# Optimization experiments

Hardware: AMD Instinct MI355X
Metric: run time of the kernel (lower is better)

## Reference

```python
import jax, jax.numpy as jnp
import numpy as np

N = 100000        # nodes
E = 1600000       # edges (N * avg_degree 16)
D_IN = 128
D_OUT = 32
OBS_T = 60        # observation_time -> decay table size 60*OBS_T = 3600
T_MAX = 60 * OBS_T


def setup_inputs() -> dict:
    key = jax.random.key(0)
    ks = jax.random.split(key, 8)
    inp = {
        "input": jax.random.normal(ks[0], (N, D_IN), dtype=jnp.float32),
        "W": jax.random.normal(ks[1], (D_IN, D_OUT), dtype=jnp.float32) * (np.sqrt(2.0) / np.sqrt(D_IN)),
        # decay weights are abs(normal(0, 0.02)) in the original; rand*0.04 is same scale
        "decay_weight1": jnp.abs(jax.random.normal(ks[2], (T_MAX, 1), dtype=jnp.float32) * 0.02),
        "decay_weight2": jnp.abs(jax.random.normal(ks[3], (T_MAX, 1), dtype=jnp.float32) * 0.02),
        "edge_row": jax.random.randint(ks[4], (E,), 0, N, dtype=jnp.int32),
        "edge_col": jax.random.randint(ks[5], (E,), 0, N, dtype=jnp.int32),
        # zero-based interval index; equals (adj_value - 1) of the original code
        "edge_time": jax.random.randint(ks[6], (E,), 0, T_MAX, dtype=jnp.int32),
        "arrive_time": jax.random.randint(ks[7], (N,), 0, T_MAX, dtype=jnp.int32),
        "observation_time": OBS_T,
    }
    return inp


def reference(input, W, decay_weight1, decay_weight2,
              edge_row, edge_col, edge_time, arrive_time, observation_time):
    n_nodes = input.shape[0]
    # h = relu(input @ W)  [N, D_OUT]
    h = jax.nn.relu(jnp.matmul(input, W))
    # one-hot(interval) @ decay_weight1 == embedding lookup  -> per-edge decay scalar
    decay = decay_weight1[edge_time, 0]                        # [E]
    # SpecialSpmm: out[i] = sum_{edges (i,j)} decay_e * h[j]  (gather-scale-scatter)
    msgs = decay[:, None] * h[edge_col]                        # [E, D_OUT]
    h_prime = jax.ops.segment_sum(msgs, edge_row, num_segments=n_nodes)
    # outlayer window decay: one-hot(60*T - arrive - 1) @ decay_weight2 == lookup
    win_idx = 60 * observation_time - arrive_time - 1          # [N] in [0, 60*T)
    h_prime = decay_weight2[win_idx, 0][:, None] * h_prime
    return h_prime
```

## Files before the change

### kernel.cpp

```cpp
#include <hip/hip_runtime.h>

#define N_NODES 100000
#define N_EDGES 1600000
#define D_IN    128
#define D_OUT   32
#define RPB     8
#define NB      (N_NODES / RPB)
#define CROWS   2048
#define NCB     49
#define FPC     (CROWS / RPB)
#define NSH     8
#define CAP_A   4500
#define DEPTH   48
#define CAPF    200
#define GEMM_BLKS ((N_NODES + 63) / 64)
#define GRID_A  2048
#define EPB_A   ((N_EDGES + GRID_A - 1) / GRID_A)

typedef __attribute__((ext_vector_type(8))) short bf16x8;
typedef __attribute__((ext_vector_type(4))) float f32x4;

__device__ inline short f2bf(float f) {
    union { float f; unsigned u; } v; v.f = f;
    unsigned r = (v.u + 0x7FFFu + ((v.u >> 16) & 1u)) >> 16;
    return (short)r;
}
__device__ inline float bf2f(unsigned short b) {
    return __uint_as_float((unsigned)b << 16);
}

union SMemGA {
    struct { short wbt[D_IN * D_OUT]; } g;
    struct { uint2 lbin[NCB][DEPTH]; int lcnt[NCB]; int gbase[NCB]; } a;
};

__global__ __launch_bounds__(256) void gemm_phaseA_kernel(
    const float* __restrict__ input, const float* __restrict__ W,
    const int* __restrict__ erow,    const int* __restrict__ ecol,
    const int* __restrict__ etime,
    unsigned short* __restrict__ h16,
    int* __restrict__ gcur,
    uint2* __restrict__ segA)
{
    __shared__ SMemGA sm;
    const int tid = threadIdx.x;

    if (blockIdx.x < GEMM_BLKS) {
        for (int i = tid; i < D_IN * D_OUT; i += 256) {
            const int k = i >> 5, c = i & 31;
            sm.g.wbt[c * D_IN + k] = f2bf(W[i]);
        }
        __syncthreads();

        const int wave = tid >> 6;
        const int lane = tid & 63;
        const int r0   = blockIdx.x * 64 + wave * 16;
        const int c16  = lane & 15;
        const int quad = lane >> 4;

        int ra = r0 + c16;
        if (ra >= N_NODES) ra = N_NODES - 1;
        const float* arow = input + (size_t)ra * D_IN;

        f32x4 acc0 = {0.f, 0.f, 0.f, 0.f};
        f32x4 acc1 = {0.f, 0.f, 0.f, 0.f};
#pragma unroll
        for (int q = 0; q < 4; ++q) {
            const float* ap = arow + q * 32 + quad * 8;
            f32x4 a0 = *(const f32x4*)(ap);
            f32x4 a1 = *(const f32x4*)(ap + 4);
            bf16x8 af;
            af[0] = f2bf(a0.x); af[1] = f2bf(a0.y); af[2] = f2bf(a0.z); af[3] = f2bf(a0.w);
            af[4] = f2bf(a1.x); af[5] = f2bf(a1.y); af[6] = f2bf(a1.z); af[7] = f2bf(a1.w);
            bf16x8 b0 = *(const bf16x8*)(sm.g.wbt + (c16)      * D_IN + q * 32 + quad * 8);
            bf16x8 b1 = *(const bf16x8*)(sm.g.wbt + (c16 + 16) * D_IN + q * 32 + quad * 8);
            acc0 = __builtin_amdgcn_mfma_f32_16x16x32_bf16(af, b0, acc0, 0, 0, 0);
            acc1 = __builtin_amdgcn_mfma_f32_16x16x32_bf16(af, b1, acc1, 0, 0, 0);
        }
#pragma unroll
        for (int i = 0; i < 4; ++i) {
            const int rr = r0 + quad * 4 + i;
            if (rr < N_NODES) {
                h16[(size_t)rr * D_OUT + c16]      = (unsigned short)f2bf(fmaxf(acc0[i], 0.f));
                h16[(size_t)rr * D_OUT + c16 + 16] = (unsigned short)f2bf(fmaxf(acc1[i], 0.f));
            }
        }
    } else {
        const int blk   = blockIdx.x - GEMM_BLKS;
        const int shard = blk & (NSH - 1);
        const int wv    = tid >> 6;
        const int ln    = tid & 63;

        if (tid < NCB) sm.a.lcnt[tid] = 0;
        __syncthreads();

        const int e_beg = blk * EPB_A;
        const int e_end = min(e_beg + EPB_A, N_EDGES);

        for (int e = e_beg + tid; e < e_end; e += 256) {
            const int row = erow[e];
            const int cb  = row >> 11;
            uint2 p;
            p.x = (unsigned)ecol[e] | ((unsigned)(row & (CROWS - 1)) << 17);
            p.y = (unsigned)etime[e];
            const int pos = atomicAdd(&sm.a.lcnt[cb], 1);
            if (pos < DEPTH) sm.a.lbin[cb][pos] = p;
            else {
                const int gp = atomicAdd(&gcur[(cb * NSH + shard) * 16], 1);
                if (gp < CAP_A) segA[(size_t)(cb * NSH + shard) * CAP_A + gp] = p;
            }
        }
        __syncthreads();

        if (tid < NCB) {
            const int c = min(sm.a.lcnt[tid], DEPTH);
            sm.a.gbase[tid] = atomicAdd(&gcur[(tid * NSH + shard) * 16], c);
        }
        __syncthreads();

        for (int bin = wv; bin < NCB; bin += 4) {
            const int c  = min(sm.a.lcnt[bin], DEPTH);
            const int gb = sm.a.gbase[bin];
            uint2* seg = segA + (size_t)(bin * NSH + shard) * CAP_A;
            for (int k = ln; k < c; k += 64)
                if (gb + k < CAP_A) seg[gb + k] = sm.a.lbin[bin][k];
        }
    }
}

__global__ __launch_bounds__(256) void phaseB_kernel(
    const int* __restrict__ gcur, const uint2* __restrict__ segA,
    int* __restrict__ fcur,
    unsigned* __restrict__ spk2)
{
    __shared__ int hist[FPC];
    __shared__ int curs[FPC];

    const int tid    = threadIdx.x;
    const int seg_id = blockIdx.x >> 1;
    const int half   = blockIdx.x & 1;
    const int cb     = seg_id >> 3;
    const int shard  = seg_id & 7;
    const int ntot   = min(gcur[(cb * NSH + shard) * 16], CAP_A);
    const int nh     = (ntot + 1) >> 1;
    const int beg    = half * nh;
    const int end    = min(ntot, beg + nh);
    const uint2* seg = segA + (size_t)(cb * NSH + shard) * CAP_A;

    hist[tid] = 0;
    __syncthreads();

    for (int i = beg + tid; i < end; i += 256)
        atomicAdd(&hist[(seg[i].x >> 20) & 255], 1);
    __syncthreads();

    {
        const int h  = hist[tid];
        const int fb = cb * FPC + tid;
        curs[tid] = (h && fb < NB) ? atomicAdd(&fcur[fb], h) : 0;
    }
    __syncthreads();

    for (int i = beg + tid; i < end; i += 256) {
        const uint2 p   = seg[i];
        const unsigned crl = (p.x >> 17) & 2047u;
        const int      fl  = crl >> 3;
        const unsigned rec = (p.x & 0x1FFFFu) | ((crl & 7u) << 17) | (p.y << 20);
        const int pos = atomicAdd(&curs[fl], 1);
        if (pos < CAPF)
            spk2[(size_t)(cb * FPC + fl) * CAPF + pos] = rec;
    }
}

__global__ __launch_bounds__(256) void bucket_reduce_kernel(
    const unsigned short* __restrict__ h16, const int* __restrict__ fcur,
    const unsigned* __restrict__ spk2, const float* __restrict__ dw1,
    const float* __restrict__ dw2, const int* __restrict__ arrive,
    const int* __restrict__ obs, float* __restrict__ out)
{
    __shared__ unsigned pk[CAPF];
    __shared__ unsigned pks[CAPF];
    __shared__ int bin[RPB];
    __shared__ int start[RPB + 1];
    __shared__ int cur[RPB];

    const int tid = threadIdx.x;
    const int b   = blockIdx.x;
    const int n   = min(fcur[b], CAPF);
    const unsigned* seg = spk2 + (size_t)b * CAPF;

    if (tid < RPB) bin[tid] = 0;
    __syncthreads();

    for (int i = tid; i < n; i += 256) {
        const unsigned p = seg[i];
        pk[i] = p;
        atomicAdd(&bin[(p >> 17) & 7], 1);
    }
    __syncthreads();

    if (tid == 0) {
        int a = 0;
#pragma unroll
        for (int r = 0; r < RPB; ++r) { start[r] = a; cur[r] = a; a += bin[r]; }
        start[RPB] = a;
    }
    __syncthreads();

    for (int i = tid; i < n; i += 256) {
        const unsigned p = pk[i];
        pks[atomicAdd(&cur[(p >> 17) & 7], 1)] = p;
    }
    __syncthreads();

    const int c = tid & 31;
    const int g = tid >> 5;
    const int T = 60 * obs[0];

    const int beg = start[g];
    const int end = start[g + 1];

    float acc = 0.f;
    int j = beg;
    for (; j + 8 <= end; j += 8) {
        float a0 = 0.f, a1 = 0.f;
#pragma unroll
        for (int u = 0; u < 8; u += 2) {
            const unsigned pa = pks[j + u];
            const unsigned pb = pks[j + u + 1];
            const float va = bf2f(h16[(size_t)(pa & 0x1FFFF) * D_OUT + c]);
            const float vb = bf2f(h16[(size_t)(pb & 0x1FFFF) * D_OUT + c]);
            a0 = fmaf(dw1[pa >> 20], va, a0);
            a1 = fmaf(dw1[pb >> 20], vb, a1);
        }
        acc += a0 + a1;
    }
    for (; j < end; ++j) {
        const unsigned p = pks[j];
        acc = fmaf(dw1[p >> 20],
                   bf2f(h16[(size_t)(p & 0x1FFFF) * D_OUT + c]), acc);
    }

    const int r = b * RPB + g;
    const float sdw = dw2[T - arrive[r] - 1];
    out[(size_t)r * D_OUT + c] = acc * sdw;
}

extern "C" void kernel_launch(void* const* d_in, const int* in_sizes, int n_in,
                              void* d_out, int out_size, void* d_ws, size_t ws_size,
                              hipStream_t stream)
{
    const float* input  = (const float*)d_in[0];
    const float* W      = (const float*)d_in[1];
    const float* dw1    = (const float*)d_in[2];
    const float* dw2    = (const float*)d_in[3];
    const int*   erow   = (const int*)d_in[4];
    const int*   ecol   = (const int*)d_in[5];
    const int*   etime  = (const int*)d_in[6];
    const int*   arrive = (const int*)d_in[7];
    const int*   obs    = (const int*)d_in[8];

    float* out = (float*)d_out;

    char* p = (char*)d_ws;
    unsigned short* h16 = (unsigned short*)p;
    p += (size_t)N_NODES * D_OUT * 2;
    p = (char*)(((size_t)p + 255) & ~(size_t)255);
    int* gcur = (int*)p;
    p += (size_t)NCB * NSH * 16 * 4;
    int* fcur = (int*)p;
    p += (size_t)NB * 4;
    p = (char*)(((size_t)p + 255) & ~(size_t)255);
    uint2* segA = (uint2*)p;
    p += (size_t)NCB * NSH * CAP_A * 8;
    p = (char*)(((size_t)p + 255) & ~(size_t)255);
    unsigned* spk2 = (unsigned*)p;

    hipMemsetAsync(gcur, 0, (size_t)(NCB * NSH * 16 + NB) * 4, stream);

    gemm_phaseA_kernel<<<GEMM_BLKS + GRID_A, 256, 0, stream>>>(
        input, W, erow, ecol, etime, h16, gcur, segA);
    phaseB_kernel<<<NCB * NSH * 2, 256, 0, stream>>>(gcur, segA, fcur, spk2);
    bucket_reduce_kernel<<<NB, 256, 0, stream>>>(
        h16, fcur, spk2, dw1, dw2, arrive, obs, out);
}
```

Before: 185.9 us.

## Replace two-phase edge binning with direct global-atomic scatter into row buckets

Removes the shared-memory coarse binning pass and the separate phaseB kernel, and instead scatters each edge straight into its 8-row bucket using one global atomicAdd per edge. GEMM and scatter blocks are now interleaved (even and odd block indices) in one launch, which drops a kernel launch and the intermediate segA buffer round trip. The cost is 1.6M global atomics spread over 12.5K counters, which may contend or serialize more than the hierarchical scheme did. GEMM_BLKS equals SCAT_BLKS (1563), so the even/odd split covers both parts exactly.

```diff
diff --git a/kernel.cpp b/kernel.cpp
--- a/kernel.cpp
+++ b/kernel.cpp
@@ -6,16 +6,10 @@
 #define D_OUT   32
 #define RPB     8
 #define NB      (N_NODES / RPB)
-#define CROWS   2048
-#define NCB     49
-#define FPC     (CROWS / RPB)
-#define NSH     8
-#define CAP_A   4500
-#define DEPTH   48
 #define CAPF    200
 #define GEMM_BLKS ((N_NODES + 63) / 64)
-#define GRID_A  2048
-#define EPB_A   ((N_EDGES + GRID_A - 1) / GRID_A)
+#define EPB_S   1024
+#define SCAT_BLKS ((N_EDGES + EPB_S - 1) / EPB_S)
 
 typedef __attribute__((ext_vector_type(8))) short bf16x8;
 typedef __attribute__((ext_vector_type(4))) float f32x4;
@@ -29,32 +23,28 @@
     return __uint_as_float((unsigned)b << 16);
 }
 
-union SMemGA {
-    struct { short wbt[D_IN * D_OUT]; } g;
-    struct { uint2 lbin[NCB][DEPTH]; int lcnt[NCB]; int gbase[NCB]; } a;
-};
-
-__global__ __launch_bounds__(256) void gemm_phaseA_kernel(
+__global__ __launch_bounds__(256) void gemm_scatter_kernel(
     const float* __restrict__ input, const float* __restrict__ W,
     const int* __restrict__ erow,    const int* __restrict__ ecol,
     const int* __restrict__ etime,
     unsigned short* __restrict__ h16,
-    int* __restrict__ gcur,
-    uint2* __restrict__ segA)
+    int* __restrict__ fcur,
+    unsigned* __restrict__ spk2)
 {
-    __shared__ SMemGA sm;
+    __shared__ short wbt[D_IN * D_OUT];
     const int tid = threadIdx.x;
 
-    if (blockIdx.x < GEMM_BLKS) {
+    if ((blockIdx.x & 1) == 0) {
+        const int gblk = blockIdx.x >> 1;
         for (int i = tid; i < D_IN * D_OUT; i += 256) {
             const int k = i >> 5, c = i & 31;
-            sm.g.wbt[c * D_IN + k] = f2bf(W[i]);
+            wbt[c * D_IN + k] = f2bf(W[i]);
         }
         __syncthreads();
 
         const int wave = tid >> 6;
         const int lane = tid & 63;
-        const int r0   = blockIdx.x * 64 + wave * 16;
+        const int r0   = gblk * 64 + wave * 16;
         const int c16  = lane & 15;
         const int quad = lane >> 4;
 
@@ -72,8 +62,8 @@
             bf16x8 af;
             af[0] = f2bf(a0.x); af[1] = f2bf(a0.y); af[2] = f2bf(a0.z); af[3] = f2bf(a0.w);
             af[4] = f2bf(a1.x); af[5] = f2bf(a1.y); af[6] = f2bf(a1.z); af[7] = f2bf(a1.w);
-            bf16x8 b0 = *(const bf16x8*)(sm.g.wbt + (c16)      * D_IN + q * 32 + quad * 8);
-            bf16x8 b1 = *(const bf16x8*)(sm.g.wbt + (c16 + 16) * D_IN + q * 32 + quad * 8);
+            bf16x8 b0 = *(const bf16x8*)(wbt + (c16)      * D_IN + q * 32 + quad * 8);
+            bf16x8 b1 = *(const bf16x8*)(wbt + (c16 + 16) * D_IN + q * 32 + quad * 8);
             acc0 = __builtin_amdgcn_mfma_f32_16x16x32_bf16(af, b0, acc0, 0, 0, 0);
             acc1 = __builtin_amdgcn_mfma_f32_16x16x32_bf16(af, b1, acc1, 0, 0, 0);
         }
@@ -86,89 +76,28 @@
             }
         }
     } else {
-        const int blk   = blockIdx.x - GEMM_BLKS;
-        const int shard = blk & (NSH - 1);
-        const int wv    = tid >> 6;
-        const int ln    = tid & 63;
-
-        if (tid < NCB) sm.a.lcnt[tid] = 0;
-        __syncthreads();
-
-        const int e_beg = blk * EPB_A;
-        const int e_end = min(e_beg + EPB_A, N_EDGES);
-
-        for (int e = e_beg + tid; e < e_end; e += 256) {
-            const int row = erow[e];
-            const int cb  = row >> 11;
-            uint2 p;
-            p.x = (unsigned)ecol[e] | ((unsigned)(row & (CROWS - 1)) << 17);
-            p.y = (unsigned)etime[e];
-            const int pos = atomicAdd(&sm.a.lcnt[cb], 1);
-            if (pos < DEPTH) sm.a.lbin[cb][pos] = p;
-            else {
-                const int gp = atomicAdd(&gcur[(cb * NSH + shard) * 16], 1);
-                if (gp < CAP_A) segA[(size_t)(cb * NSH + shard) * CAP_A + gp] = p;
+        const int sblk = blockIdx.x >> 1;
+        const int e0   = sblk * EPB_S + tid * 4;
+        if (e0 < N_EDGES) {
+            const int4 r = *(const int4*)(erow  + e0);
+            const int4 c = *(const int4*)(ecol  + e0);
+            const int4 t = *(const int4*)(etime + e0);
+            const int rows[4] = { r.x, r.y, r.z, r.w };
+            const int cols[4] = { c.x, c.y, c.z, c.w };
+            const int tms[4]  = { t.x, t.y, t.z, t.w };
+            int pos[4];
+#pragma unroll
+            for (int k = 0; k < 4; ++k)
+                pos[k] = atomicAdd(&fcur[rows[k] >> 3], 1);
+#pragma unroll
+            for (int k = 0; k < 4; ++k) {
+                const unsigned rec = (unsigned)cols[k]
+                                   | ((unsigned)(rows[k] & 7) << 17)
+                                   | ((unsigned)tms[k] << 20);
+                if (pos[k] < CAPF)
+                    spk2[(size_t)(rows[k] >> 3) * CAPF + pos[k]] = rec;
             }
         }
-        __syncthreads();
-
-        if (tid < NCB) {
-            const int c = min(sm.a.lcnt[tid], DEPTH);
-            sm.a.gbase[tid] = atomicAdd(&gcur[(tid * NSH + shard) * 16], c);
-        }
-        __syncthreads();
-
-        for (int bin = wv; bin < NCB; bin += 4) {
-            const int c  = min(sm.a.lcnt[bin], DEPTH);
-            const int gb = sm.a.gbase[bin];
-            uint2* seg = segA + (size_t)(bin * NSH + shard) * CAP_A;
-            for (int k = ln; k < c; k += 64)
-                if (gb + k < CAP_A) seg[gb + k] = sm.a.lbin[bin][k];
-        }
-    }
-}
-
-__global__ __launch_bounds__(256) void phaseB_kernel(
-    const int* __restrict__ gcur, const uint2* __restrict__ segA,
-    int* __restrict__ fcur,
-    unsigned* __restrict__ spk2)
-{
-    __shared__ int hist[FPC];
-    __shared__ int curs[FPC];
-
-    const int tid    = threadIdx.x;
-    const int seg_id = blockIdx.x >> 1;
-    const int half   = blockIdx.x & 1;
-    const int cb     = seg_id >> 3;
-    const int shard  = seg_id & 7;
-    const int ntot   = min(gcur[(cb * NSH + shard) * 16], CAP_A);
-    const int nh     = (ntot + 1) >> 1;
-    const int beg    = half * nh;
-    const int end    = min(ntot, beg + nh);
-    const uint2* seg = segA + (size_t)(cb * NSH + shard) * CAP_A;
-
-    hist[tid] = 0;
-    __syncthreads();
-
-    for (int i = beg + tid; i < end; i += 256)
-        atomicAdd(&hist[(seg[i].x >> 20) & 255], 1);
-    __syncthreads();
-
-    {
-        const int h  = hist[tid];
-        const int fb = cb * FPC + tid;
-        curs[tid] = (h && fb < NB) ? atomicAdd(&fcur[fb], h) : 0;
-    }
-    __syncthreads();
-
-    for (int i = beg + tid; i < end; i += 256) {
-        const uint2 p   = seg[i];
-        const unsigned crl = (p.x >> 17) & 2047u;
-        const int      fl  = crl >> 3;
-        const unsigned rec = (p.x & 0x1FFFFu) | ((crl & 7u) << 17) | (p.y << 20);
-        const int pos = atomicAdd(&curs[fl], 1);
-        if (pos < CAPF)
-            spk2[(size_t)(cb * FPC + fl) * CAPF + pos] = rec;
     }
 }
 
@@ -266,21 +195,15 @@
     unsigned short* h16 = (unsigned short*)p;
     p += (size_t)N_NODES * D_OUT * 2;
     p = (char*)(((size_t)p + 255) & ~(size_t)255);
-    int* gcur = (int*)p;
-    p += (size_t)NCB * NSH * 16 * 4;
     int* fcur = (int*)p;
     p += (size_t)NB * 4;
     p = (char*)(((size_t)p + 255) & ~(size_t)255);
-    uint2* segA = (uint2*)p;
-    p += (size_t)NCB * NSH * CAP_A * 8;
-    p = (char*)(((size_t)p + 255) & ~(size_t)255);
     unsigned* spk2 = (unsigned*)p;
 
-    hipMemsetAsync(gcur, 0, (size_t)(NCB * NSH * 16 + NB) * 4, stream);
-
-    gemm_phaseA_kernel<<<GEMM_BLKS + GRID_A, 256, 0, stream>>>(
-        input, W, erow, ecol, etime, h16, gcur, segA);
-    phaseB_kernel<<<NCB * NSH * 2, 256, 0, stream>>>(gcur, segA, fcur, spk2);
+    hipMemsetAsync(fcur, 0, (size_t)NB * 4, stream);
+
+    gemm_scatter_kernel<<<GEMM_BLKS + SCAT_BLKS, 256, 0, stream>>>(
+        input, W, erow, ecol, etime, h16, fcur, spk2);
     bucket_reduce_kernel<<<NB, 256, 0, stream>>>(
         h16, fcur, spk2, dw1, dw2, arrive, obs, out);
 }
```

New measurement: 217.4 us. 1.17x slower.

## Replace per-row bucket sort with LDS atomic accumulation, one warp per bucket

Applied to the files above, without the earlier changes.

The reduce kernel no longer sorts each 8-row bucket by row in shared memory. Each 32-lane group now processes a whole bucket and accumulates into an 8x32 LDS tile using shared-memory float atomics, and each block covers 8 buckets. This removes the per-block histogram, the scan and the scatter passes along with their barriers, and the new split is meant to balance load across rows. In exchange it adds LDS atomic contention when edges in a bucket share a row, and float sums now depend on atomic ordering.

```diff
diff --git a/kernel.cpp b/kernel.cpp
--- a/kernel.cpp
+++ b/kernel.cpp
@@ -16,6 +16,8 @@
 #define GEMM_BLKS ((N_NODES + 63) / 64)
 #define GRID_A  2048
 #define EPB_A   ((N_EDGES + GRID_A - 1) / GRID_A)
+#define KPB     8
+#define K3_BLKS ((NB + KPB - 1) / KPB)
 
 typedef __attribute__((ext_vector_type(8))) short bf16x8;
 typedef __attribute__((ext_vector_type(4))) float f32x4;
@@ -178,72 +180,57 @@
     const float* __restrict__ dw2, const int* __restrict__ arrive,
     const int* __restrict__ obs, float* __restrict__ out)
 {
-    __shared__ unsigned pk[CAPF];
-    __shared__ unsigned pks[CAPF];
-    __shared__ int bin[RPB];
-    __shared__ int start[RPB + 1];
-    __shared__ int cur[RPB];
+    __shared__ unsigned pk[KPB][256];
+    __shared__ float    acc[KPB * 256];
 
     const int tid = threadIdx.x;
-    const int b   = blockIdx.x;
-    const int n   = min(fcur[b], CAPF);
-    const unsigned* seg = spk2 + (size_t)b * CAPF;
-
-    if (tid < RPB) bin[tid] = 0;
-    __syncthreads();
-
-    for (int i = tid; i < n; i += 256) {
-        const unsigned p = seg[i];
-        pk[i] = p;
-        atomicAdd(&bin[(p >> 17) & 7], 1);
-    }
-    __syncthreads();
-
-    if (tid == 0) {
-        int a = 0;
-#pragma unroll
-        for (int r = 0; r < RPB; ++r) { start[r] = a; cur[r] = a; a += bin[r]; }
-        start[RPB] = a;
-    }
-    __syncthreads();
-
-    for (int i = tid; i < n; i += 256) {
-        const unsigned p = pk[i];
-        pks[atomicAdd(&cur[(p >> 17) & 7], 1)] = p;
-    }
-    __syncthreads();
-
+    const int b0  = blockIdx.x * KPB;
+
+    for (int i = tid; i < KPB * 256; i += 256) {
+        acc[i] = 0.f;
+        const int s  = i >> 8;
+        const int j  = i & 255;
+        const int bs = b0 + s;
+        if (j < CAPF && bs < NB)
+            pk[s][j] = spk2[(size_t)bs * CAPF + j];
+    }
+    __syncthreads();
+
+    const int g = tid >> 5;
     const int c = tid & 31;
-    const int g = tid >> 5;
+    const int b = b0 + g;
+    const int n = (b < NB) ? min(fcur[b], CAPF) : 0;
+    float* ag = acc + g * 256;
+    const unsigned* mypk = pk[g];
+
+    int j = 0;
+    for (; j + 4 <= n; j += 4) {
+        const unsigned r0 = mypk[j],     r1 = mypk[j + 1];
+        const unsigned r2 = mypk[j + 2], r3 = mypk[j + 3];
+        const float h0 = bf2f(h16[(size_t)(r0 & 0x1FFFF) * D_OUT + c]);
+        const float h1 = bf2f(h16[(size_t)(r1 & 0x1FFFF) * D_OUT + c]);
+        const float h2 = bf2f(h16[(size_t)(r2 & 0x1FFFF) * D_OUT + c]);
+        const float h3 = bf2f(h16[(size_t)(r3 & 0x1FFFF) * D_OUT + c]);
+        atomicAdd(&ag[((r0 >> 17) & 7) * 32 + c], dw1[r0 >> 20] * h0);
+        atomicAdd(&ag[((r1 >> 17) & 7) * 32 + c], dw1[r1 >> 20] * h1);
+        atomicAdd(&ag[((r2 >> 17) & 7) * 32 + c], dw1[r2 >> 20] * h2);
+        atomicAdd(&ag[((r3 >> 17) & 7) * 32 + c], dw1[r3 >> 20] * h3);
+    }
+    for (; j < n; ++j) {
+        const unsigned r = mypk[j];
+        const float h = bf2f(h16[(size_t)(r & 0x1FFFF) * D_OUT + c]);
+        atomicAdd(&ag[((r >> 17) & 7) * 32 + c], dw1[r >> 20] * h);
+    }
+    __syncthreads();
+
     const int T = 60 * obs[0];
-
-    const int beg = start[g];
-    const int end = start[g + 1];
-
-    float acc = 0.f;
-    int j = beg;
-    for (; j + 8 <= end; j += 8) {
-        float a0 = 0.f, a1 = 0.f;
-#pragma unroll
-        for (int u = 0; u < 8; u += 2) {
-            const unsigned pa = pks[j + u];
-            const unsigned pb = pks[j + u + 1];
-            const float va = bf2f(h16[(size_t)(pa & 0x1FFFF) * D_OUT + c]);
-            const float vb = bf2f(h16[(size_t)(pb & 0x1FFFF) * D_OUT + c]);
-            a0 = fmaf(dw1[pa >> 20], va, a0);
-            a1 = fmaf(dw1[pb >> 20], vb, a1);
-        }
-        acc += a0 + a1;
-    }
-    for (; j < end; ++j) {
-        const unsigned p = pks[j];
-        acc = fmaf(dw1[p >> 20],
-                   bf2f(h16[(size_t)(p & 0x1FFFF) * D_OUT + c]), acc);
-    }
-
-    const int r = b * RPB + g;
-    const float sdw = dw2[T - arrive[r] - 1];
-    out[(size_t)r * D_OUT + c] = acc * sdw;
+    for (int i = tid; i < KPB * 256; i += 256) {
+        const size_t flat = (size_t)b0 * 256 + i;
+        if (flat < (size_t)N_NODES * D_OUT) {
+            const int r = (int)(flat >> 5);
+            out[flat] = acc[i] * dw2[T - arrive[r] - 1];
+        }
+    }
 }
 
 extern "C" void kernel_launch(void* const* d_in, const int* in_sizes, int n_in,
@@ -281,6 +268,6 @@
     gemm_phaseA_kernel<<<GEMM_BLKS + GRID_A, 256, 0, stream>>>(
         input, W, erow, ecol, etime, h16, gcur, segA);
     phaseB_kernel<<<NCB * NSH * 2, 256, 0, stream>>>(gcur, segA, fcur, spk2);
-    bucket_reduce_kernel<<<NB, 256, 0, stream>>>(
+    bucket_reduce_kernel<<<K3_BLKS, 256, 0, stream>>>(
         h16, fcur, spk2, dw1, dw2, arrive, obs, out);
 }
```

After: 456.9 us. 146% more time.
